# Kernel tuning notes

Hardware: AMD Instinct MI355X
Metric: run time of the kernel (lower is better)

Reference implementation:

```python
import jax, jax.numpy as jnp
import numpy as np

B, S, D_IN, D_K, D_V = 4, 2048, 1024, 1024, 1024

def setup_inputs() -> dict:
    key = jax.random.key(0)
    ks = jax.random.split(key, 9)
    s = 0.02
    return {
        "query": jax.random.normal(ks[0], (B, S, D_IN), jnp.float32),
        "key_in": jax.random.normal(ks[1], (B, S, D_IN), jnp.float32),
        "value": jax.random.normal(ks[2], (B, S, D_IN), jnp.float32),
        "Wq": jax.random.normal(ks[3], (D_K, D_IN), jnp.float32) * s,
        "bq": jnp.zeros((D_K,), jnp.float32),
        "Wk": jax.random.normal(ks[4], (D_K, D_IN), jnp.float32) * s,
        "bk": jnp.zeros((D_K,), jnp.float32),
        "Wv": jax.random.normal(ks[5], (D_V, D_IN), jnp.float32) * s,
        "bv": jnp.zeros((D_V,), jnp.float32),
    }

def reference(query, key_in, value, Wq, bq, Wk, bk, Wv, bv):
    scale = D_K ** -0.5
    q = query @ Wq.T + bq          # [B,S,Dk]
    k = key_in @ Wk.T + bk         # [B,S,Dk]
    # Original quirk: self.v(value) is computed in __init__ but the forward
    # multiplies attn by the RAW value tensor, so Wv/bv are unused in the math.
    dots = jnp.einsum('bqd,bkd->bqk', q, k) * scale  # [B,S,S]
    attn = jax.nn.softmax(dots, axis=-1)
    out = jnp.einsum('bqk,bkd->bqd', attn, value)    # [B,S,D_IN]
    return out
```

## Files before the change

### kernel.cpp

```cpp
#include <hip/hip_runtime.h>
#include <hip/hip_bf16.h>
#include <stdint.h>

#define B_ 4
#define S_ 2048
#define D_ 1024

typedef __attribute__((ext_vector_type(8))) short short8;
typedef __attribute__((ext_vector_type(4))) float floatx4;

__device__ __forceinline__ unsigned short bf16_rne(float f) {
  union { float f; uint32_t u; } c; c.f = f;
  uint32_t u = c.u;
  return (unsigned short)((u + 0x7fffu + ((u >> 16) & 1u)) >> 16);
}

__device__ __forceinline__ void gl2lds16(const void* g, void* l) {
  __builtin_amdgcn_global_load_lds(
      (const __attribute__((address_space(1))) void*)g,
      (__attribute__((address_space(3))) void*)l, 16, 0, 0);
}

__global__ __launch_bounds__(256) void prep_all(
    const float* __restrict__ q, const float* __restrict__ k,
    const float* __restrict__ wq, const float* __restrict__ wk,
    const float* __restrict__ bq, const float* __restrict__ bk,
    const float* __restrict__ v,
    unsigned short* __restrict__ oq, unsigned short* __restrict__ ok,
    unsigned short* __restrict__ owq, unsigned short* __restrict__ owk,
    float* __restrict__ bias, unsigned short* __restrict__ vt) {
  __shared__ float tile[32][33];
  const int blk = blockIdx.x;
  if (blk < 18432) {
    int i = blk * 256 + threadIdx.x;
    const float* src; unsigned short* dst; int off;
    if (i < 2097152)      { src = q;  dst = oq;  off = i; }
    else if (i < 4194304) { src = k;  dst = ok;  off = i - 2097152; }
    else if (i < 4456448) { src = wq; dst = owq; off = i - 4194304; }
    else                  { src = wk; dst = owk; off = i - 4456448; }
    float4 vv = ((const float4*)src)[off];
    uint32_t p0 = (uint32_t)bf16_rne(vv.x) | ((uint32_t)bf16_rne(vv.y) << 16);
    uint32_t p1 = (uint32_t)bf16_rne(vv.z) | ((uint32_t)bf16_rne(vv.w) << 16);
    ((uint2*)dst)[off] = make_uint2(p0, p1);
  } else if (blk < 18434) {
    int j = (blk - 18432) * 256 + threadIdx.x;
    const float* src = (j < 256) ? bq : bk;
    ((float4*)bias)[j] = ((const float4*)src)[j & 255];
  } else {
    const int bi = blk - 18434;
    const int d0 = (bi & 31) * 32;
    const int s0 = ((bi >> 5) & 63) * 32;
    const int b  = bi >> 11;
    const int tx = threadIdx.x & 31, ty = threadIdx.x >> 5;
    const float* src = v + (size_t)b * S_ * D_;
#pragma unroll
    for (int i = 0; i < 4; ++i)
      tile[ty + i * 8][tx] = src[(size_t)(s0 + ty + i * 8) * D_ + d0 + tx];
    __syncthreads();
    unsigned short* dst = vt + (size_t)b * D_ * S_;
#pragma unroll
    for (int i = 0; i < 4; ++i)
      dst[(size_t)(d0 + ty + i * 8) * S_ + s0 + tx] = bf16_rne(tile[tx][ty + i * 8]);
  }
}

template <int EPI, int BM>
__global__ __launch_bounds__(256, BM == 128 ? 3 : 2) void gemm_bt(
    const unsigned short* __restrict__ A, const unsigned short* __restrict__ Bm,
    void* __restrict__ Cv, const float* __restrict__ bias,
    int N, int K, float scale,
    long long sA, long long sB, long long sC, long long sBias) {
  constexpr int IC = BM / 32;
  constexpr int AST = BM / 64;
  __shared__ unsigned short smA[2][BM * 32];
  __shared__ unsigned short smB[2][128 * 32];

  const int gx = gridDim.x, gy = gridDim.y;
  const int lin = blockIdx.x + gx * (blockIdx.y + gy * blockIdx.z);
  const int total = gx * gy * gridDim.z;
  const int g = (lin & 7) * (total >> 3) + (lin >> 3);
  const int z = g / (gx * gy);
  const int rem = g - z * (gx * gy);
  const int by = rem / gx;
  const int bx = rem - by * gx;

  const unsigned short* Ab = A + (size_t)z * sA;
  const unsigned short* Bb = Bm + (size_t)z * sB;

  const int tile_n = bx * 128;
  const int tile_m = by * BM;

  const int t = threadIdx.x;
  const int w = t >> 6;
  const int l = t & 63;
  const int wr = w >> 1, wc = w & 1;

  floatx4 acc[IC][4];
#pragma unroll
  for (int i = 0; i < IC; ++i)
#pragma unroll
    for (int j = 0; j < 4; ++j) acc[i][j] = (floatx4){0.f, 0.f, 0.f, 0.f};

  const int srow = l >> 2;
  const int scb  = ((l & 3) ^ ((l >> 3) & 3)) * 16;
  const int rm   = l & 15;
  const int kcsw = ((l >> 4) ^ ((rm >> 1) & 3)) * 16;

  for (int kt = 0; kt < K; kt += 64) {
#pragma unroll
    for (int h = 0; h < 2; ++h) {
#pragma unroll
      for (int i = 0; i < AST; ++i) {
        const int r = (i * 4 + w) * 16 + srow;
        gl2lds16((const char*)Ab + (size_t)(tile_m + r) * K * 2 + (kt + h * 32) * 2 + scb,
                 (char*)smA[h] + (i * 4 + w) * 1024);
      }
#pragma unroll
      for (int i = 0; i < 2; ++i) {
        const int r = (i * 4 + w) * 16 + srow;
        gl2lds16((const char*)Bb + (size_t)(tile_n + r) * K * 2 + (kt + h * 32) * 2 + scb,
                 (char*)smB[h] + (i * 4 + w) * 1024);
      }
    }
    __syncthreads();

#pragma unroll
    for (int h = 0; h < 2; ++h) {
      short8 bfr[4];
#pragma unroll
      for (int j = 0; j < 4; ++j)
        bfr[j] = *(const short8*)((const char*)smB[h] + (wc * 64 + j * 16 + rm) * 64 + kcsw);
#pragma unroll
      for (int i = 0; i < IC; ++i) {
        const short8 af = *(const short8*)((const char*)smA[h] +
                                           (wr * (BM / 2) + i * 16 + rm) * 64 + kcsw);
#pragma unroll
        for (int j = 0; j < 4; ++j)
          acc[i][j] = __builtin_amdgcn_mfma_f32_16x16x32_bf16(af, bfr[j], acc[i][j], 0, 0, 0);
      }
    }
    __syncthreads();
  }

#pragma unroll
  for (int i = 0; i < IC; ++i) {
#pragma unroll
    for (int j = 0; j < 4; ++j) {
      const int n = tile_n + wc * 64 + j * 16 + rm;
      const int m0 = tile_m + wr * (BM / 2) + i * 16 + (l >> 4) * 4;
      if (EPI == 0) {
        const float bv = bias[(size_t)z * sBias + n];
        unsigned short* C = (unsigned short*)Cv + (size_t)z * sC;
#pragma unroll
        for (int r = 0; r < 4; ++r)
          C[(size_t)(m0 + r) * N + n] = bf16_rne(acc[i][j][r] + bv);
      } else if (EPI == 1) {
        float* C = (float*)Cv + (size_t)z * sC;
#pragma unroll
        for (int r = 0; r < 4; ++r)
          C[(size_t)(m0 + r) * N + n] = acc[i][j][r] * scale;
      } else {
        unsigned short* C = (unsigned short*)Cv + (size_t)z * sC;
#pragma unroll
        for (int r = 0; r < 4; ++r)
          C[(size_t)(m0 + r) * N + n] = bf16_rne(acc[i][j][r] * scale);
      }
    }
  }
}

__global__ __launch_bounds__(256) void softmax_bf16(
    const unsigned short* __restrict__ logits, unsigned short* __restrict__ attn) {
  const int row = blockIdx.x;
  const int t = threadIdx.x;
  uint4 raw = *(const uint4*)(logits + (size_t)row * S_ + t * 8);
  float x[8];
  const uint32_t ru[4] = {raw.x, raw.y, raw.z, raw.w};
#pragma unroll
  for (int i = 0; i < 4; ++i) {
    union { uint32_t u; float f; } lo, hi;
    lo.u = ru[i] << 16;
    hi.u = ru[i] & 0xffff0000u;
    x[2 * i] = lo.f;
    x[2 * i + 1] = hi.f;
  }
  float m = x[0];
#pragma unroll
  for (int i = 1; i < 8; ++i) m = fmaxf(m, x[i]);
#pragma unroll
  for (int off = 32; off > 0; off >>= 1) m = fmaxf(m, __shfl_xor(m, off));
  __shared__ float sm4[4], ss4[4];
  const int wv = t >> 6, ln = t & 63;
  if (ln == 0) sm4[wv] = m;
  __syncthreads();
  m = fmaxf(fmaxf(sm4[0], sm4[1]), fmaxf(sm4[2], sm4[3]));
  float s = 0.f;
  const float LOG2E = 1.44269504088896340736f;
#pragma unroll
  for (int i = 0; i < 8; ++i) {
    x[i] = exp2f((x[i] - m) * LOG2E);
    s += x[i];
  }
#pragma unroll
  for (int off = 32; off > 0; off >>= 1) s += __shfl_xor(s, off);
  if (ln == 0) ss4[wv] = s;
  __syncthreads();
  s = ss4[0] + ss4[1] + ss4[2] + ss4[3];
  const float inv = 1.0f / s;
  uint32_t p[4];
#pragma unroll
  for (int i = 0; i < 4; ++i)
    p[i] = (uint32_t)bf16_rne(x[2 * i] * inv) |
           ((uint32_t)bf16_rne(x[2 * i + 1] * inv) << 16);
  *(uint4*)(attn + (size_t)row * S_ + t * 8) = make_uint4(p[0], p[1], p[2], p[3]);
}

extern "C" void kernel_launch(void* const* d_in, const int* in_sizes, int n_in,
                              void* d_out, int out_size, void* d_ws, size_t ws_size,
                              hipStream_t stream) {
  (void)in_sizes; (void)n_in; (void)out_size; (void)ws_size;
  const float* query  = (const float*)d_in[0];
  const float* key_in = (const float*)d_in[1];
  const float* value  = (const float*)d_in[2];
  const float* Wq     = (const float*)d_in[3];
  const float* bq     = (const float*)d_in[4];
  const float* Wk     = (const float*)d_in[5];
  const float* bk     = (const float*)d_in[6];
  float* out = (float*)d_out;

  char* ws = (char*)d_ws;
  const size_t MiB = 1024 * 1024;
  unsigned short* Xq  = (unsigned short*)(ws);
  unsigned short* Xk  = (unsigned short*)(ws + 16 * MiB);
  unsigned short* Wqb = (unsigned short*)(ws + 32 * MiB);
  unsigned short* Wkb = (unsigned short*)(ws + 34 * MiB);
  float*          Bias= (float*)(ws + 36 * MiB);
  unsigned short* Vt  = (unsigned short*)(ws + 37 * MiB);
  unsigned short* Qp  = (unsigned short*)(ws + 53 * MiB);
  unsigned short* Kp  = (unsigned short*)(ws + 69 * MiB);
  unsigned short* Lg  = (unsigned short*)(ws + 85 * MiB);
  unsigned short* At  = (unsigned short*)(ws + 117 * MiB);

  prep_all<<<26626, 256, 0, stream>>>(query, key_in, Wq, Wk, bq, bk, value,
                                      Xq, Xk, Wqb, Wkb, Bias, Vt);

  gemm_bt<0, 256><<<dim3(D_ / 128, B_ * S_ / 256, 2), 256, 0, stream>>>(
      Xq, Wqb, Qp, Bias, D_, D_, 0.f,
      (long long)B_ * S_ * D_, (long long)D_ * D_, (long long)B_ * S_ * D_, D_);

  gemm_bt<2, 256><<<dim3(S_ / 128, S_ / 256, B_), 256, 0, stream>>>(
      Qp, Kp, Lg, nullptr, S_, D_, 0.03125f,
      (long long)S_ * D_, (long long)S_ * D_, (long long)S_ * S_, 0);

  softmax_bf16<<<B_ * S_, 256, 0, stream>>>(Lg, At);

  gemm_bt<1, 128><<<dim3(D_ / 128, S_ / 128, B_), 256, 0, stream>>>(
      At, Vt, out, nullptr, D_, S_, 1.0f,
      (long long)S_ * S_, (long long)D_ * S_, (long long)S_ * D_, 0);
}
```

Measured before the change: 283.3 us.

## Add 8-wave 256x256 ping-pong GEMM kernel for projection and QK^T

```diff
diff --git a/kernel.cpp b/kernel.cpp
--- a/kernel.cpp
+++ b/kernel.cpp
@@ -169,6 +169,170 @@
   }
 }
 
+#define BAR8() { asm volatile("" ::: "memory"); __builtin_amdgcn_s_barrier(); \
+                 asm volatile("" ::: "memory"); }
+
+#define LOAD_A8(mh)                                                            \
+  _Pragma("unroll") for (int f = 0; f < 4; ++f) {                              \
+    const char* p_ = (const char*)sa + ((wr * 128 + (mh) * 64 + f * 16) * 128);\
+    a[f][0] = *(const short8*)(p_ + aoff0);                                    \
+    a[f][1] = *(const short8*)(p_ + aoff1);                                    \
+  }
+
+#define LOAD_B8(nh, barr)                                                      \
+  _Pragma("unroll") for (int j = 0; j < 2; ++j) {                              \
+    const char* p_ = (const char*)sb + ((wc * 64 + (nh) * 32 + j * 16) * 128); \
+    barr[j][0] = *(const short8*)(p_ + aoff0);                                 \
+    barr[j][1] = *(const short8*)(p_ + aoff1);                                 \
+  }
+
+#define QUAD8(mh, nh, barr)                                                    \
+  _Pragma("unroll") for (int f = 0; f < 4; ++f)                                \
+  _Pragma("unroll") for (int j = 0; j < 2; ++j)                                \
+  _Pragma("unroll") for (int kk = 0; kk < 2; ++kk)                             \
+    acc[(mh) * 4 + f][(nh) * 2 + j] =                                          \
+        __builtin_amdgcn_mfma_f32_16x16x32_bf16(                               \
+            a[f][kk], barr[j][kk], acc[(mh) * 4 + f][(nh) * 2 + j], 0, 0, 0);
+
+#define STAGE8(mat, row0, kt, ldsb)                                            \
+  _Pragma("unroll") for (int r = 0; r < 2; ++r)                                \
+    gl2lds16((const char*)(mat) +                                              \
+                 ((size_t)((row0) + r * 64 + stg_row) * K + (kt)) * 2 + stg_cb,\
+             (char*)(ldsb) + r * 8192 + w * 1024);
+
+#define STAGE8_A(buf, half, kt) \
+  STAGE8(Ab, tile_m + (half) * 128, kt, (char*)smA[buf] + (half) * 16384)
+#define STAGE8_B(buf, half, kt) \
+  STAGE8(Bb, tile_n + (half) * 128, kt, (char*)smB[buf] + (half) * 16384)
+
+template <int EPI>
+__global__ __launch_bounds__(512, 2) void gemm8_bt(
+    const unsigned short* __restrict__ A, const unsigned short* __restrict__ Bm,
+    void* __restrict__ Cv, const float* __restrict__ bias,
+    int N, int K, float scale,
+    long long sA, long long sB, long long sC, long long sBias) {
+  __shared__ unsigned short smA[2][256 * 64];
+  __shared__ unsigned short smB[2][256 * 64];
+
+  const int gx = gridDim.x, gy = gridDim.y;
+  const int lin = blockIdx.x + gx * (blockIdx.y + gy * blockIdx.z);
+  const int total = gx * gy * gridDim.z;
+  const int g = (lin & 7) * (total >> 3) + (lin >> 3);
+  const int z = g / (gx * gy);
+  const int rem = g - z * (gx * gy);
+  const int by = rem / gx;
+  const int bx = rem - by * gx;
+
+  const unsigned short* Ab = A + (size_t)z * sA;
+  const unsigned short* Bb = Bm + (size_t)z * sB;
+  const int tile_n = bx * 256;
+  const int tile_m = by * 256;
+
+  const int tid = threadIdx.x;
+  const int w = tid >> 6, l = tid & 63;
+  const int wr = w >> 2, wc = w & 3;
+
+  const int stg_row = w * 8 + (l >> 3);
+  const int stg_cb  = (((l & 7) ^ ((stg_row & 15) >> 1)) << 4);
+
+  const int rm = l & 15, kc = l >> 4;
+  const int q8 = (rm >> 1) & 7;
+  const int aoff0 = rm * 128 + ((kc ^ q8) << 4);
+  const int aoff1 = aoff0 ^ 64;
+
+  const int NT = K >> 6;
+
+  floatx4 acc[8][4];
+#pragma unroll
+  for (int i = 0; i < 8; ++i)
+#pragma unroll
+    for (int j = 0; j < 4; ++j) acc[i][j] = (floatx4){0.f, 0.f, 0.f, 0.f};
+
+  short8 a[4][2], b0[2][2], b1[2][2];
+
+  {
+    const int k1 = (NT > 1 ? 64 : 0);
+    STAGE8_A(0, 0, 0);
+    STAGE8_A(0, 1, 0);
+    STAGE8_B(0, 0, 0);
+    STAGE8_B(0, 1, 0);
+    STAGE8_B(1, 0, k1);
+    STAGE8_B(1, 1, k1);
+    STAGE8_A(1, 0, k1);
+  }
+  asm volatile("s_waitcnt vmcnt(6)" ::: "memory");
+  __builtin_amdgcn_s_barrier();
+  asm volatile("" ::: "memory");
+
+  for (int tt = 0; tt < NT; ++tt) {
+    const int cur = tt & 1, nxt = cur ^ 1;
+    const unsigned short* sa = smA[cur];
+    const unsigned short* sb = smB[cur];
+    const int ktn  = ((tt + 1 < NT) ? tt + 1 : NT - 1) * 64;
+    const int ktn2 = ((tt + 2 < NT) ? tt + 2 : NT - 1) * 64;
+
+    LOAD_A8(0)
+    LOAD_B8(0, b0)
+    STAGE8_A(nxt, 1, ktn)
+    BAR8()
+    __builtin_amdgcn_s_setprio(1);
+    QUAD8(0, 0, b0)
+    __builtin_amdgcn_s_setprio(0);
+    BAR8()
+
+    LOAD_B8(1, b1)
+    BAR8()
+    __builtin_amdgcn_s_setprio(1);
+    QUAD8(0, 1, b1)
+    __builtin_amdgcn_s_setprio(0);
+    BAR8()
+
+    LOAD_A8(1)
+    STAGE8_B(cur, 0, ktn2)
+    BAR8()
+    __builtin_amdgcn_s_setprio(1);
+    QUAD8(1, 1, b1)
+    __builtin_amdgcn_s_setprio(0);
+    BAR8()
+
+    STAGE8_B(cur, 1, ktn2)
+    STAGE8_A(cur, 0, ktn2)
+    __builtin_amdgcn_s_setprio(1);
+    QUAD8(1, 0, b0)
+    __builtin_amdgcn_s_setprio(0);
+    asm volatile("s_waitcnt vmcnt(6)" ::: "memory");
+    __builtin_amdgcn_s_barrier();
+    asm volatile("" ::: "memory");
+  }
+
+#pragma unroll
+  for (int jg = 0; jg < 4; ++jg) {
+    const int n = tile_n + wc * 64 + jg * 16 + rm;
+    float bv = 0.f;
+    if (EPI == 0) bv = bias[(size_t)z * sBias + n];
+#pragma unroll
+    for (int fg = 0; fg < 8; ++fg) {
+      const int m0 = tile_m + wr * 128 + fg * 16 + (l >> 4) * 4;
+      if (EPI == 0) {
+        unsigned short* C = (unsigned short*)Cv + (size_t)z * sC;
+#pragma unroll
+        for (int r = 0; r < 4; ++r)
+          C[(size_t)(m0 + r) * N + n] = bf16_rne(acc[fg][jg][r] + bv);
+      } else if (EPI == 1) {
+        float* C = (float*)Cv + (size_t)z * sC;
+#pragma unroll
+        for (int r = 0; r < 4; ++r)
+          C[(size_t)(m0 + r) * N + n] = acc[fg][jg][r] * scale;
+      } else {
+        unsigned short* C = (unsigned short*)Cv + (size_t)z * sC;
+#pragma unroll
+        for (int r = 0; r < 4; ++r)
+          C[(size_t)(m0 + r) * N + n] = bf16_rne(acc[fg][jg][r] * scale);
+      }
+    }
+  }
+}
+
 __global__ __launch_bounds__(256) void softmax_bf16(
     const unsigned short* __restrict__ logits, unsigned short* __restrict__ attn) {
   const int row = blockIdx.x;
@@ -244,11 +408,11 @@
   prep_all<<<26626, 256, 0, stream>>>(query, key_in, Wq, Wk, bq, bk, value,
                                       Xq, Xk, Wqb, Wkb, Bias, Vt);
 
-  gemm_bt<0, 256><<<dim3(D_ / 128, B_ * S_ / 256, 2), 256, 0, stream>>>(
+  gemm8_bt<0><<<dim3(D_ / 256, B_ * S_ / 256, 2), 512, 0, stream>>>(
       Xq, Wqb, Qp, Bias, D_, D_, 0.f,
       (long long)B_ * S_ * D_, (long long)D_ * D_, (long long)B_ * S_ * D_, D_);
 
-  gemm_bt<2, 256><<<dim3(S_ / 128, S_ / 256, B_), 256, 0, stream>>>(
+  gemm8_bt<2><<<dim3(S_ / 256, S_ / 256, B_), 512, 0, stream>>>(
       Qp, Kp, Lg, nullptr, S_, D_, 0.03125f,
       (long long)S_ * D_, (long long)S_ * D_, (long long)S_ * S_, 0);
 
```

Result: slower. 303.3 us (+7.1%).

## Fuse fp32-to-bf16 conversion of query/key into projection GEMM A-tile loads

Applied to the files above, without the earlier changes.

```diff
diff --git a/kernel.cpp b/kernel.cpp
--- a/kernel.cpp
+++ b/kernel.cpp
@@ -15,6 +15,12 @@
   return (unsigned short)((u + 0x7fffu + ((u >> 16) & 1u)) >> 16);
 }
 
+__device__ __forceinline__ uint32_t cvtpk(float a, float b) {
+  uint32_t r;
+  asm("v_cvt_pk_bf16_f32 %0, %1, %2" : "=v"(r) : "v"(a), "v"(b));
+  return r;
+}
+
 __device__ __forceinline__ void gl2lds16(const void* g, void* l) {
   __builtin_amdgcn_global_load_lds(
       (const __attribute__((address_space(1))) void*)g,
@@ -22,32 +28,15 @@
 }
 
 __global__ __launch_bounds__(256) void prep_all(
-    const float* __restrict__ q, const float* __restrict__ k,
     const float* __restrict__ wq, const float* __restrict__ wk,
     const float* __restrict__ bq, const float* __restrict__ bk,
     const float* __restrict__ v,
-    unsigned short* __restrict__ oq, unsigned short* __restrict__ ok,
     unsigned short* __restrict__ owq, unsigned short* __restrict__ owk,
     float* __restrict__ bias, unsigned short* __restrict__ vt) {
   __shared__ float tile[32][33];
   const int blk = blockIdx.x;
-  if (blk < 18432) {
-    int i = blk * 256 + threadIdx.x;
-    const float* src; unsigned short* dst; int off;
-    if (i < 2097152)      { src = q;  dst = oq;  off = i; }
-    else if (i < 4194304) { src = k;  dst = ok;  off = i - 2097152; }
-    else if (i < 4456448) { src = wq; dst = owq; off = i - 4194304; }
-    else                  { src = wk; dst = owk; off = i - 4456448; }
-    float4 vv = ((const float4*)src)[off];
-    uint32_t p0 = (uint32_t)bf16_rne(vv.x) | ((uint32_t)bf16_rne(vv.y) << 16);
-    uint32_t p1 = (uint32_t)bf16_rne(vv.z) | ((uint32_t)bf16_rne(vv.w) << 16);
-    ((uint2*)dst)[off] = make_uint2(p0, p1);
-  } else if (blk < 18434) {
-    int j = (blk - 18432) * 256 + threadIdx.x;
-    const float* src = (j < 256) ? bq : bk;
-    ((float4*)bias)[j] = ((const float4*)src)[j & 255];
-  } else {
-    const int bi = blk - 18434;
+  if (blk < 8192) {
+    const int bi = blk;
     const int d0 = (bi & 31) * 32;
     const int s0 = ((bi >> 5) & 63) * 32;
     const int b  = bi >> 11;
@@ -61,17 +50,34 @@
 #pragma unroll
     for (int i = 0; i < 4; ++i)
       dst[(size_t)(d0 + ty + i * 8) * S_ + s0 + tx] = bf16_rne(tile[tx][ty + i * 8]);
-  }
-}
-
-template <int EPI, int BM>
-__global__ __launch_bounds__(256, BM == 128 ? 3 : 2) void gemm_bt(
-    const unsigned short* __restrict__ A, const unsigned short* __restrict__ Bm,
-    void* __restrict__ Cv, const float* __restrict__ bias,
-    int N, int K, float scale,
-    long long sA, long long sB, long long sC, long long sBias) {
+  } else if (blk < 8194) {
+    int j = (blk - 8192) * 256 + threadIdx.x;
+    const float* src = (j < 256) ? bq : bk;
+    ((float4*)bias)[j] = ((const float4*)src)[j & 255];
+  } else {
+    const int stride = 512 * 256;
+    for (int unit = (blk - 8194) * 256 + threadIdx.x; unit < 262144; unit += stride) {
+      const float* src; unsigned short* dst; int off;
+      if (unit < 131072) { src = wq; dst = owq; off = unit; }
+      else               { src = wk; dst = owk; off = unit - 131072; }
+      float4 v0 = ((const float4*)src)[2 * off];
+      float4 v1 = ((const float4*)src)[2 * off + 1];
+      uint4 o;
+      o.x = (uint32_t)bf16_rne(v0.x) | ((uint32_t)bf16_rne(v0.y) << 16);
+      o.y = (uint32_t)bf16_rne(v0.z) | ((uint32_t)bf16_rne(v0.w) << 16);
+      o.z = (uint32_t)bf16_rne(v1.x) | ((uint32_t)bf16_rne(v1.y) << 16);
+      o.w = (uint32_t)bf16_rne(v1.z) | ((uint32_t)bf16_rne(v1.w) << 16);
+      ((uint4*)dst)[off] = o;
+    }
+  }
+}
+
+__global__ __launch_bounds__(256, 2) void gemm_proj(
+    const float* __restrict__ Aq, const float* __restrict__ Ak,
+    const unsigned short* __restrict__ Bm, unsigned short* __restrict__ C,
+    const float* __restrict__ bias) {
+  constexpr int BM = 256;
   constexpr int IC = BM / 32;
-  constexpr int AST = BM / 64;
   __shared__ unsigned short smA[2][BM * 32];
   __shared__ unsigned short smB[2][128 * 32];
 
@@ -84,8 +90,8 @@
   const int by = rem / gx;
   const int bx = rem - by * gx;
 
-  const unsigned short* Ab = A + (size_t)z * sA;
-  const unsigned short* Bb = Bm + (size_t)z * sB;
+  const float* Ab = z ? Ak : Aq;
+  const unsigned short* Bb = Bm + (size_t)z * (D_ * D_);
 
   const int tile_n = bx * 128;
   const int tile_m = by * BM;
@@ -106,6 +112,111 @@
   const int rm   = l & 15;
   const int kcsw = ((l >> 4) ^ ((rm >> 1) & 3)) * 16;
 
+  for (int kt = 0; kt < 1024; kt += 64) {
+    float4 fa[2][4][2];
+#pragma unroll
+    for (int h = 0; h < 2; ++h) {
+#pragma unroll
+      for (int i = 0; i < 2; ++i) {
+        const int r = (i * 4 + w) * 16 + srow;
+        gl2lds16((const char*)Bb + (size_t)(tile_n + r) * 1024 * 2 + (kt + h * 32) * 2 + scb,
+                 (char*)smB[h] + (i * 4 + w) * 1024);
+      }
+#pragma unroll
+      for (int i = 0; i < 4; ++i) {
+        const int r = (i * 4 + w) * 16 + srow;
+        const float* gp = Ab + (size_t)(tile_m + r) * 1024 + (kt + h * 32) + (scb >> 1);
+        fa[h][i][0] = *(const float4*)gp;
+        fa[h][i][1] = *(const float4*)(gp + 4);
+      }
+    }
+#pragma unroll
+    for (int h = 0; h < 2; ++h)
+#pragma unroll
+      for (int i = 0; i < 4; ++i) {
+        uint4 o;
+        o.x = cvtpk(fa[h][i][0].x, fa[h][i][0].y);
+        o.y = cvtpk(fa[h][i][0].z, fa[h][i][0].w);
+        o.z = cvtpk(fa[h][i][1].x, fa[h][i][1].y);
+        o.w = cvtpk(fa[h][i][1].z, fa[h][i][1].w);
+        *(uint4*)((char*)smA[h] + (i * 4 + w) * 1024 + (l << 4)) = o;
+      }
+    __syncthreads();
+
+#pragma unroll
+    for (int h = 0; h < 2; ++h) {
+      short8 bfr[4];
+#pragma unroll
+      for (int j = 0; j < 4; ++j)
+        bfr[j] = *(const short8*)((const char*)smB[h] + (wc * 64 + j * 16 + rm) * 64 + kcsw);
+#pragma unroll
+      for (int i = 0; i < IC; ++i) {
+        const short8 af = *(const short8*)((const char*)smA[h] +
+                                           (wr * (BM / 2) + i * 16 + rm) * 64 + kcsw);
+#pragma unroll
+        for (int j = 0; j < 4; ++j)
+          acc[i][j] = __builtin_amdgcn_mfma_f32_16x16x32_bf16(af, bfr[j], acc[i][j], 0, 0, 0);
+      }
+    }
+    __syncthreads();
+  }
+
+#pragma unroll
+  for (int i = 0; i < IC; ++i) {
+#pragma unroll
+    for (int j = 0; j < 4; ++j) {
+      const int n = tile_n + wc * 64 + j * 16 + rm;
+      const int m0 = tile_m + wr * (BM / 2) + i * 16 + (l >> 4) * 4;
+      const float bv = bias[(size_t)z * D_ + n];
+#pragma unroll
+      for (int r = 0; r < 4; ++r)
+        C[(size_t)z * (B_ * S_ * D_) + (size_t)(m0 + r) * D_ + n] =
+            bf16_rne(acc[i][j][r] + bv);
+    }
+  }
+}
+
+template <int EPI, int BM>
+__global__ __launch_bounds__(256, BM == 128 ? 3 : 2) void gemm_bt(
+    const unsigned short* __restrict__ A, const unsigned short* __restrict__ Bm,
+    void* __restrict__ Cv, int N, int K, float scale,
+    long long sA, long long sB, long long sC) {
+  constexpr int IC = BM / 32;
+  constexpr int AST = BM / 64;
+  __shared__ unsigned short smA[2][BM * 32];
+  __shared__ unsigned short smB[2][128 * 32];
+
+  const int gx = gridDim.x, gy = gridDim.y;
+  const int lin = blockIdx.x + gx * (blockIdx.y + gy * blockIdx.z);
+  const int total = gx * gy * gridDim.z;
+  const int g = (lin & 7) * (total >> 3) + (lin >> 3);
+  const int z = g / (gx * gy);
+  const int rem = g - z * (gx * gy);
+  const int by = rem / gx;
+  const int bx = rem - by * gx;
+
+  const unsigned short* Ab = A + (size_t)z * sA;
+  const unsigned short* Bb = Bm + (size_t)z * sB;
+
+  const int tile_n = bx * 128;
+  const int tile_m = by * BM;
+
+  const int t = threadIdx.x;
+  const int w = t >> 6;
+  const int l = t & 63;
+  const int wr = w >> 1, wc = w & 1;
+
+  floatx4 acc[IC][4];
+#pragma unroll
+  for (int i = 0; i < IC; ++i)
+#pragma unroll
+    for (int j = 0; j < 4; ++j) acc[i][j] = (floatx4){0.f, 0.f, 0.f, 0.f};
+
+  const int srow = l >> 2;
+  const int scb  = ((l & 3) ^ ((l >> 3) & 3)) * 16;
+  const int rm   = l & 15;
+  const int kcsw = ((l >> 4) ^ ((rm >> 1) & 3)) * 16;
+
   for (int kt = 0; kt < K; kt += 64) {
 #pragma unroll
     for (int h = 0; h < 2; ++h) {
@@ -148,13 +259,7 @@
     for (int j = 0; j < 4; ++j) {
       const int n = tile_n + wc * 64 + j * 16 + rm;
       const int m0 = tile_m + wr * (BM / 2) + i * 16 + (l >> 4) * 4;
-      if (EPI == 0) {
-        const float bv = bias[(size_t)z * sBias + n];
-        unsigned short* C = (unsigned short*)Cv + (size_t)z * sC;
-#pragma unroll
-        for (int r = 0; r < 4; ++r)
-          C[(size_t)(m0 + r) * N + n] = bf16_rne(acc[i][j][r] + bv);
-      } else if (EPI == 1) {
+      if (EPI == 1) {
         float* C = (float*)Cv + (size_t)z * sC;
 #pragma unroll
         for (int r = 0; r < 4; ++r)
@@ -169,11 +274,10 @@
   }
 }
 
-__global__ __launch_bounds__(256) void softmax_bf16(
-    const unsigned short* __restrict__ logits, unsigned short* __restrict__ attn) {
+__global__ __launch_bounds__(256) void softmax_bf16(unsigned short* data) {
   const int row = blockIdx.x;
   const int t = threadIdx.x;
-  uint4 raw = *(const uint4*)(logits + (size_t)row * S_ + t * 8);
+  uint4 raw = *(const uint4*)(data + (size_t)row * S_ + t * 8);
   float x[8];
   const uint32_t ru[4] = {raw.x, raw.y, raw.z, raw.w};
 #pragma unroll
@@ -212,7 +316,7 @@
   for (int i = 0; i < 4; ++i)
     p[i] = (uint32_t)bf16_rne(x[2 * i] * inv) |
            ((uint32_t)bf16_rne(x[2 * i + 1] * inv) << 16);
-  *(uint4*)(attn + (size_t)row * S_ + t * 8) = make_uint4(p[0], p[1], p[2], p[3]);
+  *(uint4*)(data + (size_t)row * S_ + t * 8) = make_uint4(p[0], p[1], p[2], p[3]);
 }
 
 extern "C" void kernel_launch(void* const* d_in, const int* in_sizes, int n_in,
@@ -230,31 +334,27 @@
 
   char* ws = (char*)d_ws;
   const size_t MiB = 1024 * 1024;
-  unsigned short* Xq  = (unsigned short*)(ws);
-  unsigned short* Xk  = (unsigned short*)(ws + 16 * MiB);
-  unsigned short* Wqb = (unsigned short*)(ws + 32 * MiB);
-  unsigned short* Wkb = (unsigned short*)(ws + 34 * MiB);
-  float*          Bias= (float*)(ws + 36 * MiB);
-  unsigned short* Vt  = (unsigned short*)(ws + 37 * MiB);
-  unsigned short* Qp  = (unsigned short*)(ws + 53 * MiB);
-  unsigned short* Kp  = (unsigned short*)(ws + 69 * MiB);
-  unsigned short* Lg  = (unsigned short*)(ws + 85 * MiB);
-  unsigned short* At  = (unsigned short*)(ws + 117 * MiB);
-
-  prep_all<<<26626, 256, 0, stream>>>(query, key_in, Wq, Wk, bq, bk, value,
-                                      Xq, Xk, Wqb, Wkb, Bias, Vt);
-
-  gemm_bt<0, 256><<<dim3(D_ / 128, B_ * S_ / 256, 2), 256, 0, stream>>>(
-      Xq, Wqb, Qp, Bias, D_, D_, 0.f,
-      (long long)B_ * S_ * D_, (long long)D_ * D_, (long long)B_ * S_ * D_, D_);
+  unsigned short* Wqb = (unsigned short*)(ws);
+  unsigned short* Wkb = (unsigned short*)(ws + 2 * MiB);
+  float*          Bias= (float*)(ws + 4 * MiB);
+  unsigned short* Vt  = (unsigned short*)(ws + 5 * MiB);
+  unsigned short* Qp  = (unsigned short*)(ws + 21 * MiB);
+  unsigned short* Kp  = (unsigned short*)(ws + 37 * MiB);
+  unsigned short* Lg  = (unsigned short*)(ws + 53 * MiB);
+
+  prep_all<<<8706, 256, 0, stream>>>(Wq, Wk, bq, bk, value,
+                                     Wqb, Wkb, Bias, Vt);
+
+  gemm_proj<<<dim3(D_ / 128, B_ * S_ / 256, 2), 256, 0, stream>>>(
+      query, key_in, Wqb, Qp, Bias);
 
   gemm_bt<2, 256><<<dim3(S_ / 128, S_ / 256, B_), 256, 0, stream>>>(
-      Qp, Kp, Lg, nullptr, S_, D_, 0.03125f,
-      (long long)S_ * D_, (long long)S_ * D_, (long long)S_ * S_, 0);
-
-  softmax_bf16<<<B_ * S_, 256, 0, stream>>>(Lg, At);
+      Qp, Kp, Lg, S_, D_, 0.03125f,
+      (long long)S_ * D_, (long long)S_ * D_, (long long)S_ * S_);
+
+  softmax_bf16<<<B_ * S_, 256, 0, stream>>>(Lg);
 
   gemm_bt<1, 128><<<dim3(D_ / 128, S_ / 128, B_), 256, 0, stream>>>(
-      At, Vt, out, nullptr, D_, S_, 1.0f,
-      (long long)S_ * S_, (long long)D_ * S_, (long long)S_ * D_, 0);
-}
+      Lg, Vt, out, D_, S_, 1.0f,
+      (long long)S_ * S_, (long long)D_ * S_, (long long)S_ * D_);
+}
```

New measurement: 298.7 us. 5.4% more time.
